# Kernel optimization log

Hardware: AMD Instinct MI355X
Metric: run time of the kernel (lower is better)

The kernel has to match this reference:

```python
import math
import jax, jax.numpy as jnp
import numpy as np

B, T, C = 8, 4096, 1024
N_HEAD = 16
HS = C // N_HEAD  # head_size = 64


def _keep_indices(T):
    # Faithful Python/math replication of the row-gather index list.
    a = math.ceil(T / 4)
    keep = [T - 1 - x for x in range(a)]
    keep += [T - 1 - math.ceil(3 / a * (x - a) ** 2 + a) for x in range(a, math.ceil(T / 2))]
    return np.array(list(reversed(keep)), dtype=np.int32)  # [K] = [ceil(T/2)]


def setup_inputs() -> dict:
    key = jax.random.key(0)
    ks = jax.random.split(key, 7)
    s = 1.0 / math.sqrt(C)  # torch Linear default init scale
    return {
        "x": jax.random.normal(ks[0], (B, T, C), dtype=jnp.float32),
        "Wq": jax.random.uniform(ks[1], (HS, C), jnp.float32, -s, s),
        "bq": jax.random.uniform(ks[2], (HS,), jnp.float32, -s, s),
        "Wk": jax.random.uniform(ks[3], (HS, C), jnp.float32, -s, s),
        "bk": jax.random.uniform(ks[4], (HS,), jnp.float32, -s, s),
        "Wv": jax.random.uniform(ks[5], (HS, C), jnp.float32, -s, s),
        "bv": jax.random.uniform(ks[6], (HS,), jnp.float32, -s, s),
    }


def reference(x, Wq, bq, Wk, bk, Wv, bv):
    Bx, Tx, Cx = x.shape
    keep = jnp.asarray(_keep_indices(Tx))                    # [K], static
    q = x @ Wq.T + bq                                        # [B,T,hs]
    k = x @ Wk.T + bk                                        # [B,T,hs]
    v = x @ Wv.T + bv                                        # [B,T,hs]
    # Original computes full q@k^T then gathers rows; gathering q rows first
    # is the same math without materializing [B,T,T].
    qg = q[:, keep, :]                                       # [B,K,hs]
    att = jnp.einsum('bkd,btd->bkt', qg, k) * (Cx ** -0.5)   # scale by n_embd, per source
    # fade_tril = tril[keep, :T]: row i allows positions j <= keep[i]
    mask = jnp.arange(Tx)[None, :] <= keep[:, None]          # [K,T]
    att = jnp.where(mask[None], att, -jnp.inf)
    att = jax.nn.softmax(att, axis=-1)
    # dropout p=0.0 -> identity
    out = jnp.einsum('bkt,btd->bkd', att, v)                 # [B,K,hs]
    return out
```

## Files before the change

### kernel.cpp

```cpp
#include <hip/hip_runtime.h>
#include <hip/hip_bf16.h>

typedef __attribute__((ext_vector_type(8))) short s8v;
typedef __attribute__((ext_vector_type(4))) short s4v;
typedef __attribute__((ext_vector_type(4))) float f4v;

#define B_   8
#define T_   4096
#define C_   1024
#define HS_  64
#define K2_  2048

#define SLAB_ 1040

__device__ __forceinline__ int keep_of(int i) {
    if (i >= 1024) return 2048 + i;
    int d = 1023 - i;
    return 3071 - ((3 * d * d + 1023) >> 10);
}

__device__ __forceinline__ short bf16_bits(float f) {
    union { __hip_bfloat16 h; short s; } u;
    u.h = __float2bfloat16(f);
    return u.s;
}

__device__ __forceinline__ s8v cvt8f(const float* p) {
    const f4v a = *(const f4v*)p;
    const f4v b = *(const f4v*)(p + 4);
    s8v r;
    r[0] = bf16_bits(a[0]); r[1] = bf16_bits(a[1]);
    r[2] = bf16_bits(a[2]); r[3] = bf16_bits(a[3]);
    r[4] = bf16_bits(b[0]); r[5] = bf16_bits(b[1]);
    r[6] = bf16_bits(b[2]); r[7] = bf16_bits(b[3]);
    return r;
}

__device__ __forceinline__ void gload_lds16(const void* g, void* l) {
    __builtin_amdgcn_global_load_lds(
        (__attribute__((address_space(1))) void*)(g),
        (__attribute__((address_space(3))) void*)(l), 16, 0, 0);
}

__global__ __launch_bounds__(256) void wcvt_kernel(
    const float* __restrict__ Wq, const float* __restrict__ Wk,
    const float* __restrict__ Wv, short* __restrict__ Wb)
{
    const int idx = (blockIdx.x * 256 + threadIdx.x) * 8;
    const int mat = idx >> 16;
    const int off = idx & 65535;
    const float* src = (mat == 0) ? Wq : (mat == 1) ? Wk : Wv;
    *(s8v*)(Wb + idx) = cvt8f(src + off);
}

__global__ __launch_bounds__(256) void qkv_kernel(
    const float* __restrict__ x,
    const short* __restrict__ Wb,
    const float* __restrict__ bq, const float* __restrict__ bk,
    const float* __restrict__ bv,
    __hip_bfloat16* __restrict__ Qo, __hip_bfloat16* __restrict__ Ko,
    __hip_bfloat16* __restrict__ Vt)
{
    __shared__ __align__(16) char smem[40960];
    float* xs  = (float*)smem;
    short* wsm = (short*)(smem + 16384);

    const int tid  = threadIdx.x;
    const int wave = tid >> 6;
    const int lane = tid & 63;
    const int l16  = lane & 15;
    const int quad = lane >> 4;
    const int row0 = blockIdx.x * 64;

    f4v acc[3][4];
    #pragma unroll
    for (int m = 0; m < 3; ++m)
        #pragma unroll
        for (int mt = 0; mt < 4; ++mt) {
            acc[m][mt][0] = 0.f; acc[m][mt][1] = 0.f;
            acc[m][mt][2] = 0.f; acc[m][mt][3] = 0.f;
        }

    int xrow[4], xoff[4];
    #pragma unroll
    for (int i = 0; i < 4; ++i) {
        const int f = 256 * i + tid;
        xrow[i] = f >> 4;
        xoff[i] = ((f & 15) ^ (xrow[i] & 7)) * 4;
    }
    int wrow[6], woff[6];
    #pragma unroll
    for (int i = 0; i < 6; ++i) {
        const int f = 256 * i + tid;
        wrow[i] = f >> 3;
        woff[i] = ((f & 7) ^ (wrow[i] & 7)) * 8;
    }

    for (int k0 = 0; k0 < C_; k0 += 64) {
        __syncthreads();
        #pragma unroll
        for (int i = 0; i < 4; ++i)
            gload_lds16(x + (size_t)(row0 + xrow[i]) * C_ + k0 + xoff[i],
                        (char*)xs + (256 * i + tid) * 16);
        #pragma unroll
        for (int i = 0; i < 6; ++i)
            gload_lds16(Wb + (size_t)wrow[i] * C_ + k0 + woff[i],
                        (char*)wsm + (256 * i + tid) * 16);
        __syncthreads();

        #pragma unroll
        for (int kh = 0; kh < 2; ++kh) {
            s8v a[4];
            #pragma unroll
            for (int mt = 0; mt < 4; ++mt) {
                const int r   = mt * 16 + l16;
                const int ch0 = kh * 8 + quad * 2;
                const float* p0 = xs + r * 64 + ((ch0    ) ^ (r & 7)) * 4;
                const float* p1 = xs + r * 64 + ((ch0 + 1) ^ (r & 7)) * 4;
                const f4v u = *(const f4v*)p0;
                const f4v v = *(const f4v*)p1;
                s8v af;
                af[0] = bf16_bits(u[0]); af[1] = bf16_bits(u[1]);
                af[2] = bf16_bits(u[2]); af[3] = bf16_bits(u[3]);
                af[4] = bf16_bits(v[0]); af[5] = bf16_bits(v[1]);
                af[6] = bf16_bits(v[2]); af[7] = bf16_bits(v[3]);
                a[mt] = af;
            }
            #pragma unroll
            for (int m = 0; m < 3; ++m) {
                const int wr = m * 64 + wave * 16 + l16;
                const int ch = kh * 4 + quad;
                const s8v bf = *(const s8v*)(wsm + wr * 64 + ((ch ^ (wr & 7)) * 8));
                #pragma unroll
                for (int mt = 0; mt < 4; ++mt)
                    acc[m][mt] = __builtin_amdgcn_mfma_f32_16x16x32_bf16(a[mt], bf, acc[m][mt], 0, 0, 0);
            }
        }
    }

    const int wc = wave * 16 + l16;
    const float bqv = bq[wc], bkv = bk[wc], bvv = bv[wc];
    #pragma unroll
    for (int mt = 0; mt < 4; ++mt) {
        const int rbase = row0 + mt * 16 + quad * 4;
        #pragma unroll
        for (int r = 0; r < 4; ++r) {
            Qo[(size_t)(rbase + r) * HS_ + wc] = __float2bfloat16(acc[0][mt][r] + bqv);
            Ko[(size_t)(rbase + r) * HS_ + wc] = __float2bfloat16(acc[1][mt][r] + bkv);
        }
        s4v vp;
        #pragma unroll
        for (int r = 0; r < 4; ++r) vp[r] = bf16_bits(acc[2][mt][r] + bvv);
        const int bb = rbase >> 12;
        const int tt = rbase & (T_ - 1);
        *(s4v*)(Vt + ((size_t)(bb * HS_ + wc)) * T_ + tt) = vp;
    }
}

__global__ __launch_bounds__(256) void attn_kernel(
    const __hip_bfloat16* __restrict__ Qo,
    const __hip_bfloat16* __restrict__ Ko,
    const __hip_bfloat16* __restrict__ Vt,
    float* __restrict__ pws)
{
    __shared__ __align__(16) char smem[17408];
    float* mL = (float*)smem;
    float* mO = (float*)(smem + 256);

    const int b    = blockIdx.x & 7;
    const int s    = blockIdx.x >> 3;
    const int qb   = 127 - (s >> 1);
    const int half = s & 1;
    const int tid  = threadIdx.x;
    const int wave = tid >> 6;
    const int lane = tid & 63;
    const int l16  = lane & 15;
    const int quad = lane >> 4;

    short* pw0 = (short*)smem + wave * 2048;

    const int qt = keep_of(qb * 16 + l16);
    const __hip_bfloat16* qrow = Qo + ((size_t)(b * T_ + qt)) * HS_;
    const s8v aq0 = *(const s8v*)(qrow + quad * 8);
    const s8v aq1 = *(const s8v*)(qrow + 32 + quad * 8);

    int keepr[4];
    #pragma unroll
    for (int r = 0; r < 4; ++r) keepr[r] = keep_of(qb * 16 + quad * 4 + r);

    const int kmin   = keep_of(qb * 16);
    const int tmax   = keep_of(qb * 16 + 15);
    const int ntiles = (tmax >> 6) + 1;

    f4v accO[4];
    #pragma unroll
    for (int j = 0; j < 4; ++j) { accO[j][0]=0.f; accO[j][1]=0.f; accO[j][2]=0.f; accO[j][3]=0.f; }
    float l_p[4] = {0.f, 0.f, 0.f, 0.f};

    const __hip_bfloat16* kbase = Ko + (size_t)b * T_ * HS_;
    const __hip_bfloat16* vbase = Vt + (size_t)b * HS_ * T_;

    s8v kreg[8], vreg[8];

    int tt = half + 2 * wave;
    if (tt < ntiles) {
        const int t0 = tt << 6;
        #pragma unroll
        for (int jn = 0; jn < 4; ++jn) {
            const __hip_bfloat16* kr = kbase + (size_t)(t0 + jn * 16 + l16) * HS_ + quad * 8;
            kreg[jn * 2    ] = *(const s8v*)(kr);
            kreg[jn * 2 + 1] = *(const s8v*)(kr + 32);
        }
        #pragma unroll
        for (int jd = 0; jd < 4; ++jd) {
            const __hip_bfloat16* vr = vbase + (size_t)(jd * 16 + l16) * T_ + t0 + quad * 8;
            vreg[jd * 2    ] = *(const s8v*)(vr);
            vreg[jd * 2 + 1] = *(const s8v*)(vr + 32);
        }
    }

    for (; tt < ntiles; tt += 8) {
        const int t0 = tt << 6;
        const int tn = tt + 8;
        short* pw = pw0 + ((tt >> 3) & 1) * 1024;

        f4v s4[4];
        #pragma unroll
        for (int jn = 0; jn < 4; ++jn) {
            f4v z; z[0]=0.f; z[1]=0.f; z[2]=0.f; z[3]=0.f;
            z = __builtin_amdgcn_mfma_f32_16x16x32_bf16(aq0, kreg[jn * 2    ], z, 0, 0, 0);
            z = __builtin_amdgcn_mfma_f32_16x16x32_bf16(aq1, kreg[jn * 2 + 1], z, 0, 0, 0);
            s4[jn] = z;
        }

        if (tn < ntiles) {
            const int t0n = tn << 6;
            #pragma unroll
            for (int jn = 0; jn < 4; ++jn) {
                const __hip_bfloat16* kr = kbase + (size_t)(t0n + jn * 16 + l16) * HS_ + quad * 8;
                kreg[jn * 2    ] = *(const s8v*)(kr);
                kreg[jn * 2 + 1] = *(const s8v*)(kr + 32);
            }
        }

        if (t0 + 63 <= kmin) {
            #pragma unroll
            for (int jn = 0; jn < 4; ++jn) {
                const int t = jn * 16 + l16;
                const int chunk = t >> 3;
                #pragma unroll
                for (int r = 0; r < 4; ++r) {
                    const float p = __expf(s4[jn][r] * 0.03125f);
                    l_p[r] += p;
                    const int m = quad * 4 + r;
                    pw[m * 64 + ((chunk ^ (m & 7)) * 8) + (t & 7)] = bf16_bits(p);
                }
            }
        } else {
            #pragma unroll
            for (int jn = 0; jn < 4; ++jn) {
                const int t = jn * 16 + l16;
                const int valid_t = t0 + t;
                const int chunk = t >> 3;
                #pragma unroll
                for (int r = 0; r < 4; ++r) {
                    const float e = __expf(s4[jn][r] * 0.03125f);
                    const float p = (valid_t <= keepr[r]) ? e : 0.0f;
                    l_p[r] += p;
                    const int m = quad * 4 + r;
                    pw[m * 64 + ((chunk ^ (m & 7)) * 8) + (t & 7)] = bf16_bits(p);
                }
            }
        }
        const s8v ap0 = *(const s8v*)(pw + l16 * 64 + ((quad    ) ^ (l16 & 7)) * 8);
        const s8v ap1 = *(const s8v*)(pw + l16 * 64 + ((quad + 4) ^ (l16 & 7)) * 8);

        #pragma unroll
        for (int jd = 0; jd < 4; ++jd) {
            accO[jd] = __builtin_amdgcn_mfma_f32_16x16x32_bf16(ap0, vreg[jd * 2    ], accO[jd], 0, 0, 0);
            accO[jd] = __builtin_amdgcn_mfma_f32_16x16x32_bf16(ap1, vreg[jd * 2 + 1], accO[jd], 0, 0, 0);
        }

        if (tn < ntiles) {
            const int t0n = tn << 6;
            #pragma unroll
            for (int jd = 0; jd < 4; ++jd) {
                const __hip_bfloat16* vr = vbase + (size_t)(jd * 16 + l16) * T_ + t0n + quad * 8;
                vreg[jd * 2    ] = *(const s8v*)(vr);
                vreg[jd * 2 + 1] = *(const s8v*)(vr + 32);
            }
        }
    }

    #pragma unroll
    for (int off = 1; off < 16; off <<= 1)
        #pragma unroll
        for (int r = 0; r < 4; ++r) l_p[r] += __shfl_xor(l_p[r], off);

    __syncthreads();
    #pragma unroll
    for (int r = 0; r < 4; ++r) {
        const int row = quad * 4 + r;
        if (l16 == 0) mL[wave * 16 + row] = l_p[r];
        #pragma unroll
        for (int jd = 0; jd < 4; ++jd)
            mO[wave * 1024 + row * 64 + jd * 16 + l16] = accO[jd][r];
    }
    __syncthreads();

    {
        const int row = tid >> 4;
        const int col = (tid & 15) * 4;
        float L = 0.f;
        #pragma unroll
        for (int w = 0; w < 4; ++w) L += mL[w * 16 + row];
        f4v o; o[0]=0.f; o[1]=0.f; o[2]=0.f; o[3]=0.f;
        #pragma unroll
        for (int w = 0; w < 4; ++w) {
            const f4v ow = *(const f4v*)(mO + w * 1024 + row * 64 + col);
            #pragma unroll
            for (int j = 0; j < 4; ++j) o[j] += ow[j];
        }
        float* slab = pws + ((size_t)((b * 128 + qb) * 2 + half)) * SLAB_;
        *(f4v*)(slab + row * 64 + col) = o;
        if ((tid & 15) == 0) slab[1024 + row] = L;
    }
}

__global__ __launch_bounds__(256) void merge_kernel(
    const float* __restrict__ pws, float* __restrict__ out)
{
    const int b   = blockIdx.x & 7;
    const int qb  = blockIdx.x >> 3;
    const int tid = threadIdx.x;
    const int row = tid >> 4;
    const int col = (tid & 15) * 4;

    const float* s0 = pws + ((size_t)((b * 128 + qb) * 2    )) * SLAB_;
    const float* s1 = pws + ((size_t)((b * 128 + qb) * 2 + 1)) * SLAB_;
    const f4v o0 = *(const f4v*)(s0 + row * 64 + col);
    const f4v o1 = *(const f4v*)(s1 + row * 64 + col);
    const float inv = 1.0f / (s0[1024 + row] + s1[1024 + row]);
    f4v o;
    #pragma unroll
    for (int j = 0; j < 4; ++j) o[j] = (o0[j] + o1[j]) * inv;
    *(f4v*)(out + ((size_t)(b * K2_ + qb * 16 + row)) * HS_ + col) = o;
}

extern "C" void kernel_launch(void* const* d_in, const int* in_sizes, int n_in,
                              void* d_out, int out_size, void* d_ws, size_t ws_size,
                              hipStream_t stream) {
    (void)in_sizes; (void)n_in; (void)out_size; (void)ws_size;
    const float* x  = (const float*)d_in[0];
    const float* Wq = (const float*)d_in[1];
    const float* bq = (const float*)d_in[2];
    const float* Wk = (const float*)d_in[3];
    const float* bk = (const float*)d_in[4];
    const float* Wv = (const float*)d_in[5];
    const float* bv = (const float*)d_in[6];

    __hip_bfloat16* Qo = (__hip_bfloat16*)d_ws;
    __hip_bfloat16* Ko = Qo + (size_t)B_ * T_ * HS_;
    __hip_bfloat16* Vt = Ko + (size_t)B_ * T_ * HS_;
    short*          Wb = (short*)(Vt + (size_t)B_ * HS_ * T_);
    float*          pws = (float*)(Wb + 196608);
    float* o = (float*)d_out;

    wcvt_kernel<<<dim3(96), dim3(256), 0, stream>>>(Wq, Wk, Wv, Wb);
    qkv_kernel<<<dim3((B_ * T_) / 64), dim3(256), 0, stream>>>(
        x, Wb, bq, bk, bv, Qo, Ko, Vt);
    attn_kernel<<<dim3(B_ * 256), dim3(256), 0, stream>>>(Qo, Ko, Vt, pws);
    merge_kernel<<<dim3(B_ * 128), dim3(256), 0, stream>>>(pws, o);
}
```

Measured before the change: 298.2 us.

## Pair light and heavy query blocks per workgroup and drop merge kernel

```diff
diff --git a/kernel.cpp b/kernel.cpp
--- a/kernel.cpp
+++ b/kernel.cpp
@@ -10,8 +10,6 @@
 #define C_   1024
 #define HS_  64
 #define K2_  2048
-
-#define SLAB_ 1040
 
 __device__ __forceinline__ int keep_of(int i) {
     if (i >= 1024) return 2048 + i;
@@ -161,16 +159,14 @@
     const __hip_bfloat16* __restrict__ Qo,
     const __hip_bfloat16* __restrict__ Ko,
     const __hip_bfloat16* __restrict__ Vt,
-    float* __restrict__ pws)
+    float* __restrict__ out)
 {
     __shared__ __align__(16) char smem[17408];
     float* mL = (float*)smem;
     float* mO = (float*)(smem + 256);
 
     const int b    = blockIdx.x & 7;
-    const int s    = blockIdx.x >> 3;
-    const int qb   = 127 - (s >> 1);
-    const int half = s & 1;
+    const int pp   = blockIdx.x >> 3;
     const int tid  = threadIdx.x;
     const int wave = tid >> 6;
     const int lane = tid & 63;
@@ -179,172 +175,159 @@
 
     short* pw0 = (short*)smem + wave * 2048;
 
-    const int qt = keep_of(qb * 16 + l16);
-    const __hip_bfloat16* qrow = Qo + ((size_t)(b * T_ + qt)) * HS_;
-    const s8v aq0 = *(const s8v*)(qrow + quad * 8);
-    const s8v aq1 = *(const s8v*)(qrow + 32 + quad * 8);
-
-    int keepr[4];
-    #pragma unroll
-    for (int r = 0; r < 4; ++r) keepr[r] = keep_of(qb * 16 + quad * 4 + r);
-
-    const int kmin   = keep_of(qb * 16);
-    const int tmax   = keep_of(qb * 16 + 15);
-    const int ntiles = (tmax >> 6) + 1;
-
-    f4v accO[4];
-    #pragma unroll
-    for (int j = 0; j < 4; ++j) { accO[j][0]=0.f; accO[j][1]=0.f; accO[j][2]=0.f; accO[j][3]=0.f; }
-    float l_p[4] = {0.f, 0.f, 0.f, 0.f};
-
     const __hip_bfloat16* kbase = Ko + (size_t)b * T_ * HS_;
     const __hip_bfloat16* vbase = Vt + (size_t)b * HS_ * T_;
 
-    s8v kreg[8], vreg[8];
-
-    int tt = half + 2 * wave;
-    if (tt < ntiles) {
-        const int t0 = tt << 6;
-        #pragma unroll
-        for (int jn = 0; jn < 4; ++jn) {
-            const __hip_bfloat16* kr = kbase + (size_t)(t0 + jn * 16 + l16) * HS_ + quad * 8;
-            kreg[jn * 2    ] = *(const s8v*)(kr);
-            kreg[jn * 2 + 1] = *(const s8v*)(kr + 32);
-        }
-        #pragma unroll
-        for (int jd = 0; jd < 4; ++jd) {
-            const __hip_bfloat16* vr = vbase + (size_t)(jd * 16 + l16) * T_ + t0 + quad * 8;
-            vreg[jd * 2    ] = *(const s8v*)(vr);
-            vreg[jd * 2 + 1] = *(const s8v*)(vr + 32);
-        }
-    }
-
-    for (; tt < ntiles; tt += 8) {
-        const int t0 = tt << 6;
-        const int tn = tt + 8;
-        short* pw = pw0 + ((tt >> 3) & 1) * 1024;
-
-        f4v s4[4];
-        #pragma unroll
-        for (int jn = 0; jn < 4; ++jn) {
-            f4v z; z[0]=0.f; z[1]=0.f; z[2]=0.f; z[3]=0.f;
-            z = __builtin_amdgcn_mfma_f32_16x16x32_bf16(aq0, kreg[jn * 2    ], z, 0, 0, 0);
-            z = __builtin_amdgcn_mfma_f32_16x16x32_bf16(aq1, kreg[jn * 2 + 1], z, 0, 0, 0);
-            s4[jn] = z;
-        }
-
-        if (tn < ntiles) {
-            const int t0n = tn << 6;
+    #pragma unroll 1
+    for (int which = 0; which < 2; ++which) {
+        const int qb = which ? (63 - pp) : (64 + pp);
+
+        const int qt = keep_of(qb * 16 + l16);
+        const __hip_bfloat16* qrow = Qo + ((size_t)(b * T_ + qt)) * HS_;
+        const s8v aq0 = *(const s8v*)(qrow + quad * 8);
+        const s8v aq1 = *(const s8v*)(qrow + 32 + quad * 8);
+
+        int keepr[4];
+        #pragma unroll
+        for (int r = 0; r < 4; ++r) keepr[r] = keep_of(qb * 16 + quad * 4 + r);
+
+        const int kmin   = keep_of(qb * 16);
+        const int tmax   = keep_of(qb * 16 + 15);
+        const int ntiles = (tmax >> 6) + 1;
+
+        f4v accO[4];
+        #pragma unroll
+        for (int j = 0; j < 4; ++j) { accO[j][0]=0.f; accO[j][1]=0.f; accO[j][2]=0.f; accO[j][3]=0.f; }
+        float l_p[4] = {0.f, 0.f, 0.f, 0.f};
+
+        s8v kreg[8], vreg[8];
+
+        int tt = wave;
+        if (tt < ntiles) {
+            const int t0 = tt << 6;
             #pragma unroll
             for (int jn = 0; jn < 4; ++jn) {
-                const __hip_bfloat16* kr = kbase + (size_t)(t0n + jn * 16 + l16) * HS_ + quad * 8;
+                const __hip_bfloat16* kr = kbase + (size_t)(t0 + jn * 16 + l16) * HS_ + quad * 8;
                 kreg[jn * 2    ] = *(const s8v*)(kr);
                 kreg[jn * 2 + 1] = *(const s8v*)(kr + 32);
             }
-        }
-
-        if (t0 + 63 <= kmin) {
-            #pragma unroll
-            for (int jn = 0; jn < 4; ++jn) {
-                const int t = jn * 16 + l16;
-                const int chunk = t >> 3;
-                #pragma unroll
-                for (int r = 0; r < 4; ++r) {
-                    const float p = __expf(s4[jn][r] * 0.03125f);
-                    l_p[r] += p;
-                    const int m = quad * 4 + r;
-                    pw[m * 64 + ((chunk ^ (m & 7)) * 8) + (t & 7)] = bf16_bits(p);
-                }
-            }
-        } else {
-            #pragma unroll
-            for (int jn = 0; jn < 4; ++jn) {
-                const int t = jn * 16 + l16;
-                const int valid_t = t0 + t;
-                const int chunk = t >> 3;
-                #pragma unroll
-                for (int r = 0; r < 4; ++r) {
-                    const float e = __expf(s4[jn][r] * 0.03125f);
-                    const float p = (valid_t <= keepr[r]) ? e : 0.0f;
-                    l_p[r] += p;
-                    const int m = quad * 4 + r;
-                    pw[m * 64 + ((chunk ^ (m & 7)) * 8) + (t & 7)] = bf16_bits(p);
-                }
-            }
-        }
-        const s8v ap0 = *(const s8v*)(pw + l16 * 64 + ((quad    ) ^ (l16 & 7)) * 8);
-        const s8v ap1 = *(const s8v*)(pw + l16 * 64 + ((quad + 4) ^ (l16 & 7)) * 8);
-
-        #pragma unroll
-        for (int jd = 0; jd < 4; ++jd) {
-            accO[jd] = __builtin_amdgcn_mfma_f32_16x16x32_bf16(ap0, vreg[jd * 2    ], accO[jd], 0, 0, 0);
-            accO[jd] = __builtin_amdgcn_mfma_f32_16x16x32_bf16(ap1, vreg[jd * 2 + 1], accO[jd], 0, 0, 0);
-        }
-
-        if (tn < ntiles) {
-            const int t0n = tn << 6;
             #pragma unroll
             for (int jd = 0; jd < 4; ++jd) {
-                const __hip_bfloat16* vr = vbase + (size_t)(jd * 16 + l16) * T_ + t0n + quad * 8;
+                const __hip_bfloat16* vr = vbase + (size_t)(jd * 16 + l16) * T_ + t0 + quad * 8;
                 vreg[jd * 2    ] = *(const s8v*)(vr);
                 vreg[jd * 2 + 1] = *(const s8v*)(vr + 32);
             }
         }
-    }
-
-    #pragma unroll
-    for (int off = 1; off < 16; off <<= 1)
-        #pragma unroll
-        for (int r = 0; r < 4; ++r) l_p[r] += __shfl_xor(l_p[r], off);
-
-    __syncthreads();
-    #pragma unroll
-    for (int r = 0; r < 4; ++r) {
-        const int row = quad * 4 + r;
-        if (l16 == 0) mL[wave * 16 + row] = l_p[r];
-        #pragma unroll
-        for (int jd = 0; jd < 4; ++jd)
-            mO[wave * 1024 + row * 64 + jd * 16 + l16] = accO[jd][r];
-    }
-    __syncthreads();
-
-    {
-        const int row = tid >> 4;
-        const int col = (tid & 15) * 4;
-        float L = 0.f;
-        #pragma unroll
-        for (int w = 0; w < 4; ++w) L += mL[w * 16 + row];
-        f4v o; o[0]=0.f; o[1]=0.f; o[2]=0.f; o[3]=0.f;
-        #pragma unroll
-        for (int w = 0; w < 4; ++w) {
-            const f4v ow = *(const f4v*)(mO + w * 1024 + row * 64 + col);
-            #pragma unroll
-            for (int j = 0; j < 4; ++j) o[j] += ow[j];
-        }
-        float* slab = pws + ((size_t)((b * 128 + qb) * 2 + half)) * SLAB_;
-        *(f4v*)(slab + row * 64 + col) = o;
-        if ((tid & 15) == 0) slab[1024 + row] = L;
-    }
-}
-
-__global__ __launch_bounds__(256) void merge_kernel(
-    const float* __restrict__ pws, float* __restrict__ out)
-{
-    const int b   = blockIdx.x & 7;
-    const int qb  = blockIdx.x >> 3;
-    const int tid = threadIdx.x;
-    const int row = tid >> 4;
-    const int col = (tid & 15) * 4;
-
-    const float* s0 = pws + ((size_t)((b * 128 + qb) * 2    )) * SLAB_;
-    const float* s1 = pws + ((size_t)((b * 128 + qb) * 2 + 1)) * SLAB_;
-    const f4v o0 = *(const f4v*)(s0 + row * 64 + col);
-    const f4v o1 = *(const f4v*)(s1 + row * 64 + col);
-    const float inv = 1.0f / (s0[1024 + row] + s1[1024 + row]);
-    f4v o;
-    #pragma unroll
-    for (int j = 0; j < 4; ++j) o[j] = (o0[j] + o1[j]) * inv;
-    *(f4v*)(out + ((size_t)(b * K2_ + qb * 16 + row)) * HS_ + col) = o;
+
+        for (; tt < ntiles; tt += 4) {
+            const int t0 = tt << 6;
+            const int tn = tt + 4;
+            short* pw = pw0 + ((tt >> 2) & 1) * 1024;
+
+            f4v s4[4];
+            #pragma unroll
+            for (int jn = 0; jn < 4; ++jn) {
+                f4v z; z[0]=0.f; z[1]=0.f; z[2]=0.f; z[3]=0.f;
+                z = __builtin_amdgcn_mfma_f32_16x16x32_bf16(aq0, kreg[jn * 2    ], z, 0, 0, 0);
+                z = __builtin_amdgcn_mfma_f32_16x16x32_bf16(aq1, kreg[jn * 2 + 1], z, 0, 0, 0);
+                s4[jn] = z;
+            }
+
+            if (tn < ntiles) {
+                const int t0n = tn << 6;
+                #pragma unroll
+                for (int jn = 0; jn < 4; ++jn) {
+                    const __hip_bfloat16* kr = kbase + (size_t)(t0n + jn * 16 + l16) * HS_ + quad * 8;
+                    kreg[jn * 2    ] = *(const s8v*)(kr);
+                    kreg[jn * 2 + 1] = *(const s8v*)(kr + 32);
+                }
+            }
+
+            if (t0 + 63 <= kmin) {
+                #pragma unroll
+                for (int jn = 0; jn < 4; ++jn) {
+                    const int t = jn * 16 + l16;
+                    const int chunk = t >> 3;
+                    #pragma unroll
+                    for (int r = 0; r < 4; ++r) {
+                        const float p = __expf(s4[jn][r] * 0.03125f);
+                        l_p[r] += p;
+                        const int m = quad * 4 + r;
+                        pw[m * 64 + ((chunk ^ (m & 7)) * 8) + (t & 7)] = bf16_bits(p);
+                    }
+                }
+            } else {
+                #pragma unroll
+                for (int jn = 0; jn < 4; ++jn) {
+                    const int t = jn * 16 + l16;
+                    const int valid_t = t0 + t;
+                    const int chunk = t >> 3;
+                    #pragma unroll
+                    for (int r = 0; r < 4; ++r) {
+                        const float e = __expf(s4[jn][r] * 0.03125f);
+                        const float p = (valid_t <= keepr[r]) ? e : 0.0f;
+                        l_p[r] += p;
+                        const int m = quad * 4 + r;
+                        pw[m * 64 + ((chunk ^ (m & 7)) * 8) + (t & 7)] = bf16_bits(p);
+                    }
+                }
+            }
+            const s8v ap0 = *(const s8v*)(pw + l16 * 64 + ((quad    ) ^ (l16 & 7)) * 8);
+            const s8v ap1 = *(const s8v*)(pw + l16 * 64 + ((quad + 4) ^ (l16 & 7)) * 8);
+
+            #pragma unroll
+            for (int jd = 0; jd < 4; ++jd) {
+                accO[jd] = __builtin_amdgcn_mfma_f32_16x16x32_bf16(ap0, vreg[jd * 2    ], accO[jd], 0, 0, 0);
+                accO[jd] = __builtin_amdgcn_mfma_f32_16x16x32_bf16(ap1, vreg[jd * 2 + 1], accO[jd], 0, 0, 0);
+            }
+
+            if (tn < ntiles) {
+                const int t0n = tn << 6;
+                #pragma unroll
+                for (int jd = 0; jd < 4; ++jd) {
+                    const __hip_bfloat16* vr = vbase + (size_t)(jd * 16 + l16) * T_ + t0n + quad * 8;
+                    vreg[jd * 2    ] = *(const s8v*)(vr);
+                    vreg[jd * 2 + 1] = *(const s8v*)(vr + 32);
+                }
+            }
+        }
+
+        #pragma unroll
+        for (int off = 1; off < 16; off <<= 1)
+            #pragma unroll
+            for (int r = 0; r < 4; ++r) l_p[r] += __shfl_xor(l_p[r], off);
+
+        __syncthreads();
+        #pragma unroll
+        for (int r = 0; r < 4; ++r) {
+            const int row = quad * 4 + r;
+            if (l16 == 0) mL[wave * 16 + row] = l_p[r];
+            #pragma unroll
+            for (int jd = 0; jd < 4; ++jd)
+                mO[wave * 1024 + row * 64 + jd * 16 + l16] = accO[jd][r];
+        }
+        __syncthreads();
+
+        {
+            const int row = tid >> 4;
+            const int col = (tid & 15) * 4;
+            float L = 0.f;
+            #pragma unroll
+            for (int w = 0; w < 4; ++w) L += mL[w * 16 + row];
+            const float inv = 1.0f / L;
+            f4v o; o[0]=0.f; o[1]=0.f; o[2]=0.f; o[3]=0.f;
+            #pragma unroll
+            for (int w = 0; w < 4; ++w) {
+                const f4v ow = *(const f4v*)(mO + w * 1024 + row * 64 + col);
+                #pragma unroll
+                for (int j = 0; j < 4; ++j) o[j] += ow[j];
+            }
+            #pragma unroll
+            for (int j = 0; j < 4; ++j) o[j] *= inv;
+            *(f4v*)(out + ((size_t)(b * K2_ + qb * 16 + row)) * HS_ + col) = o;
+        }
+        __syncthreads();
+    }
 }
 
 extern "C" void kernel_launch(void* const* d_in, const int* in_sizes, int n_in,
@@ -363,12 +346,10 @@
     __hip_bfloat16* Ko = Qo + (size_t)B_ * T_ * HS_;
     __hip_bfloat16* Vt = Ko + (size_t)B_ * T_ * HS_;
     short*          Wb = (short*)(Vt + (size_t)B_ * HS_ * T_);
-    float*          pws = (float*)(Wb + 196608);
     float* o = (float*)d_out;
 
     wcvt_kernel<<<dim3(96), dim3(256), 0, stream>>>(Wq, Wk, Wv, Wb);
     qkv_kernel<<<dim3((B_ * T_) / 64), dim3(256), 0, stream>>>(
         x, Wb, bq, bk, bv, Qo, Ko, Vt);
-    attn_kernel<<<dim3(B_ * 256), dim3(256), 0, stream>>>(Qo, Ko, Vt, pws);
-    merge_kernel<<<dim3(B_ * 128), dim3(256), 0, stream>>>(pws, o);
-}
+    attn_kernel<<<dim3(512), dim3(256), 0, stream>>>(Qo, Ko, Vt, o);
+}
```

Result: no change. 295.7 us (-0.8%).
